# Optimization experiments

Hardware: AMD Instinct MI355X
Metric: run time of the kernel (lower is better)

Reference implementation:

```python
import jax, jax.numpy as jnp
import numpy as np

DIM = 128
LAYERS = 3
N_NODES = 50000
N_EDGES = 640000
LN_EPS = 1e-5


def setup_inputs() -> dict:
    key = jax.random.key(0)
    ks = jax.random.split(key, 10)
    s = 1.0 / np.sqrt(DIM)
    x = jax.random.normal(ks[0], (N_NODES, DIM), dtype=jnp.float32)
    edge_index = jax.random.randint(ks[1], (2, N_EDGES), 0, N_NODES, dtype=jnp.int64)
    in_w = jax.random.uniform(ks[2], (DIM, DIM), jnp.float32, -s, s)
    in_b = jax.random.uniform(ks[3], (DIM,), jnp.float32, -s, s)
    w1 = jax.random.uniform(ks[4], (LAYERS, DIM, DIM), jnp.float32, -s, s)
    b1 = jax.random.uniform(ks[5], (LAYERS, DIM), jnp.float32, -s, s)
    w2 = jax.random.uniform(ks[6], (LAYERS, DIM, DIM), jnp.float32, -s, s)
    b2 = jax.random.uniform(ks[7], (LAYERS, DIM), jnp.float32, -s, s)
    ln_g = jnp.ones((LAYERS, DIM), jnp.float32)
    ln_b = jnp.zeros((LAYERS, DIM), jnp.float32)
    return {"x": x, "edge_index": edge_index, "in_w": in_w, "in_b": in_b,
            "w1": w1, "b1": b1, "w2": w2, "b2": b2, "ln_g": ln_g, "ln_b": ln_b}


def _layer_norm(z, g, b):
    mu = jnp.mean(z, axis=-1, keepdims=True)
    var = jnp.mean(jnp.square(z - mu), axis=-1, keepdims=True)
    return (z - mu) * jax.lax.rsqrt(var + LN_EPS) * g + b


def reference(x, edge_index, in_w, in_b, w1, b1, w2, b2, ln_g, ln_b):
    src, dst = edge_index[0], edge_index[1]
    n = x.shape[0]
    # degree is identical every layer in the original; compute once (same math)
    deg = jax.ops.segment_sum(jnp.ones(dst.shape, x.dtype), dst, num_segments=n)
    deg = jnp.maximum(deg, 1.0)[:, None]  # [N,1]
    h = x @ in_w + in_b  # [N,D]
    for i in range(w1.shape[0]):
        m = jax.ops.segment_sum(h[src], dst, num_segments=n) / deg  # gather+scatter
        mlp = jax.nn.relu(m @ w1[i] + b1[i]) @ w2[i] + b2[i]
        h = _layer_norm(h + mlp, ln_g[i], ln_b[i])
    return h
```

## Files before the change

kernel.cpp:

```cpp
#include <hip/hip_runtime.h>
#include <hip/hip_fp8.h>

#define DIM 128
#define LN_EPS 1e-5f

typedef __attribute__((ext_vector_type(8))) short s16x8;
typedef __attribute__((ext_vector_type(4))) float f32x4;
typedef __attribute__((ext_vector_type(2))) float f32x2;
typedef __attribute__((ext_vector_type(4))) unsigned int u32x4;
typedef __attribute__((ext_vector_type(2))) unsigned int u32x2;

__device__ __forceinline__ unsigned short f2bf(float f) {
    unsigned u = __float_as_uint(f);
    unsigned r = u + 0x7fffu + ((u >> 16) & 1u);
    return (unsigned short)(r >> 16);
}
__device__ __forceinline__ float bf2f(unsigned short b) {
    return __uint_as_float(((unsigned)b) << 16);
}
__device__ __forceinline__ unsigned char f2fp8(float f) {
    return (unsigned char)__hip_cvt_float_to_fp8(f, __HIP_SATFINITE, __HIP_E4M3);
}
__device__ __forceinline__ void acc_fp8x4(float* a, unsigned v) {
    f32x2 lo = __builtin_amdgcn_cvt_pk_f32_fp8(v, false);
    f32x2 hi = __builtin_amdgcn_cvt_pk_f32_fp8(v, true);
    a[0] += lo[0]; a[1] += lo[1]; a[2] += hi[0]; a[3] += hi[1];
}


__global__ void count_deg(const int* __restrict__ dst, int E, int* __restrict__ counts) {
    int i = blockIdx.x * 256 + threadIdx.x;
    if (i < E) atomicAdd(&counts[dst[i]], 1);
}

__global__ __launch_bounds__(256) void scan_partials(const int* __restrict__ counts, int n,
                                                     int* __restrict__ bsum) {
    int base = blockIdx.x * 1024 + threadIdx.x * 4;
    int s = 0;
#pragma unroll
    for (int j = 0; j < 4; ++j) {
        int i = base + j;
        if (i < n) s += counts[i];
    }
#pragma unroll
    for (int off = 32; off > 0; off >>= 1) s += __shfl_xor(s, off, 64);
    __shared__ int wsum[4];
    int lane = threadIdx.x & 63, wid = threadIdx.x >> 6;
    if (lane == 0) wsum[wid] = s;
    __syncthreads();
    if (threadIdx.x == 0) bsum[blockIdx.x] = wsum[0] + wsum[1] + wsum[2] + wsum[3];
}

__global__ __launch_bounds__(64) void scan_bsums(const int* __restrict__ bsum,
                                                 int* __restrict__ bofs, int nb,
                                                 int* __restrict__ rowptr, int N, int E) {
    int lane = threadIdx.x;
    int carry = 0;
    for (int base = 0; base < nb; base += 64) {
        int v = (base + lane < nb) ? bsum[base + lane] : 0;
        int incl = v;
#pragma unroll
        for (int off = 1; off < 64; off <<= 1) {
            int t = __shfl_up(incl, off, 64);
            if (lane >= off) incl += t;
        }
        if (base + lane < nb) bofs[base + lane] = carry + incl - v;
        carry += __shfl(incl, 63, 64);
    }
    if (lane == 0) rowptr[N] = E;
}

__global__ __launch_bounds__(256) void scan_final(const int* __restrict__ counts, int n,
                                                  const int* __restrict__ bofs,
                                                  int* __restrict__ rowptr,
                                                  int* __restrict__ cursor,
                                                  float* __restrict__ dinv) {
    int base = blockIdx.x * 1024 + threadIdx.x * 4;
    int v[4];
#pragma unroll
    for (int j = 0; j < 4; ++j) {
        int i = base + j;
        v[j] = (i < n) ? counts[i] : 0;
    }
    int tsum = v[0] + v[1] + v[2] + v[3];
    int lane = threadIdx.x & 63, wid = threadIdx.x >> 6;
    int incl = tsum;
#pragma unroll
    for (int off = 1; off < 64; off <<= 1) {
        int t = __shfl_up(incl, off, 64);
        if (lane >= off) incl += t;
    }
    __shared__ int wsum[4];
    if (lane == 63) wsum[wid] = incl;
    __syncthreads();
    int wofs = 0;
    for (int w = 0; w < 4; ++w)
        if (w < wid) wofs += wsum[w];
    int excl = bofs[blockIdx.x] + wofs + (incl - tsum);
#pragma unroll
    for (int j = 0; j < 4; ++j) {
        int i = base + j;
        if (i < n) {
            rowptr[i] = excl;
            cursor[i] = excl;
            dinv[i] = 1.0f / (float)((v[j] > 1) ? v[j] : 1);
            excl += v[j];
        }
    }
}

__global__ void fill_csr(const int* __restrict__ src, const int* __restrict__ dst, int E,
                         int* __restrict__ cursor, int* __restrict__ srcidx) {
    int i = blockIdx.x * 256 + threadIdx.x;
    if (i < E) {
        int p = atomicAdd(&cursor[dst[i]], 1);
        srcidx[p] = src[i];
    }
}


__global__ __launch_bounds__(256) void cvt_weights(const float* __restrict__ in_w,
                                                   const float* __restrict__ w1,
                                                   const float* __restrict__ w2,
                                                   unsigned short* __restrict__ wt, int L) {
    int mat = blockIdx.x >> 3, part = blockIdx.x & 7;
    const float* src;
    if (mat == 0) src = in_w;
    else if (mat <= L) src = w1 + (size_t)(mat - 1) * DIM * DIM;
    else src = w2 + (size_t)(mat - 1 - L) * DIM * DIM;
    unsigned short* dst = wt + (size_t)mat * DIM * DIM;
    int base = part * 2048 + threadIdx.x;
#pragma unroll
    for (int j = 0; j < 8; ++j) {
        int i = base + j * 256;
        int k = i >> 7, n = i & 127;
        dst[n * DIM + k] = f2bf(src[i]);
    }
}


__global__ __launch_bounds__(256) void gemm_bias_mfma(const float* __restrict__ x,
                                                      const unsigned short* __restrict__ Wt,
                                                      const float* __restrict__ bias,
                                                      unsigned short* __restrict__ hb,
                                                      unsigned char* __restrict__ h8, int N) {
    int tid = threadIdx.x;
    int s = tid >> 6, lane = tid & 63;
    int quad = lane >> 4, l16 = lane & 15;
    int r0 = blockIdx.x * 16;
    int cs = s * 32;
    int arow = r0 + l16;
    bool av = arow < N;

    f32x4 acc[2];
    acc[0] = (f32x4){0.f, 0.f, 0.f, 0.f};
    acc[1] = (f32x4){0.f, 0.f, 0.f, 0.f};

    const float4* xp = (const float4*)(x + ((size_t)(av ? arow : 0) << 7)) + quad * 2;
#pragma unroll
    for (int k0 = 0; k0 < 128; k0 += 32) {
        s16x8 a = {0, 0, 0, 0, 0, 0, 0, 0};
        if (av) {
            float4 f0 = xp[k0 / 4];
            float4 f1 = xp[k0 / 4 + 1];
            a[0] = (short)f2bf(f0.x); a[1] = (short)f2bf(f0.y);
            a[2] = (short)f2bf(f0.z); a[3] = (short)f2bf(f0.w);
            a[4] = (short)f2bf(f1.x); a[5] = (short)f2bf(f1.y);
            a[6] = (short)f2bf(f1.z); a[7] = (short)f2bf(f1.w);
        }
        s16x8 b0 = *(const s16x8*)(Wt + ((size_t)(cs + l16) << 7) + quad * 8 + k0);
        s16x8 b1 = *(const s16x8*)(Wt + ((size_t)(cs + 16 + l16) << 7) + quad * 8 + k0);
        acc[0] = __builtin_amdgcn_mfma_f32_16x16x32_bf16(a, b0, acc[0], 0, 0, 0);
        acc[1] = __builtin_amdgcn_mfma_f32_16x16x32_bf16(a, b1, acc[1], 0, 0, 0);
    }

#pragma unroll
    for (int c = 0; c < 2; ++c) {
        int col = cs + c * 16 + l16;
        float bv = bias[col];
#pragma unroll
        for (int reg = 0; reg < 4; ++reg) {
            int grow = r0 + quad * 4 + reg;
            if (grow < N) {
                float o = acc[c][reg] + bv;
                hb[((size_t)grow << 7) + col] = f2bf(o);
                h8[((size_t)grow << 7) + col] = f2fp8(o);
            }
        }
    }
}


__global__ __launch_bounds__(256) void agg_mlp_ln(const unsigned short* __restrict__ hin,
                                                  const unsigned char* __restrict__ h8in,
                                                  const int* __restrict__ rowptr,
                                                  const int* __restrict__ srcidx,
                                                  const float* __restrict__ dinv,
                                                  const unsigned short* __restrict__ W1t,
                                                  const float* __restrict__ B1,
                                                  const unsigned short* __restrict__ W2t,
                                                  const float* __restrict__ B2,
                                                  const float* __restrict__ G,
                                                  const float* __restrict__ Bb,
                                                  unsigned short* __restrict__ hout,
                                                  unsigned char* __restrict__ h8out,
                                                  float* __restrict__ out_f32, int N) {
    __shared__ unsigned short M[16][132];
    __shared__ unsigned short P[16][132];
    __shared__ float s1p[4][16], s2p[4][16];

    int tid = threadIdx.x;
    int s = tid >> 6, lane = tid & 63;
    int quad = lane >> 4, l16 = lane & 15;
    int g = lane >> 2, li = lane & 3;
    int r0 = blockIdx.x * 16;
    int cs = s * 32;

    int nd = r0 + g;
    bool nv = nd < N;
    int e  = nv ? rowptr[nd] : 0;
    int ee = nv ? rowptr[nd + 1] : 0;

    float a0[8] = {0, 0, 0, 0, 0, 0, 0, 0};
    float a1[8] = {0, 0, 0, 0, 0, 0, 0, 0};
    const unsigned char* hsl = h8in + cs + li * 8;

    while (__any(e < ee)) {
        int myidx = (e + li < ee) ? srcidx[e + li] : 0;
        int i0 = __shfl(myidx, (g << 2) | 0, 64);
        int i1 = __shfl(myidx, (g << 2) | 1, 64);
        int i2 = __shfl(myidx, (g << 2) | 2, 64);
        int i3 = __shfl(myidx, (g << 2) | 3, 64);
        bool p0 = e < ee, p1 = e + 1 < ee, p2 = e + 2 < ee, p3 = e + 3 < ee;
        u32x2 v0, v1, v2, v3;
        if (p0) v0 = *(const u32x2*)(hsl + ((size_t)i0 << 7));
        if (p1) v1 = *(const u32x2*)(hsl + ((size_t)i1 << 7));
        if (p2) v2 = *(const u32x2*)(hsl + ((size_t)i2 << 7));
        if (p3) v3 = *(const u32x2*)(hsl + ((size_t)i3 << 7));
        if (p0) { acc_fp8x4(a0,     v0[0]); acc_fp8x4(a0 + 4, v0[1]); }
        if (p1) { acc_fp8x4(a1,     v1[0]); acc_fp8x4(a1 + 4, v1[1]); }
        if (p2) { acc_fp8x4(a0,     v2[0]); acc_fp8x4(a0 + 4, v2[1]); }
        if (p3) { acc_fp8x4(a1,     v3[0]); acc_fp8x4(a1 + 4, v3[1]); }
        e += 4;
    }

    {
        float di = nv ? dinv[nd] : 0.f;
        u32x4 o;
#pragma unroll
        for (int j = 0; j < 4; ++j) {
            unsigned lo = f2bf((a0[2 * j]     + a1[2 * j])     * di);
            unsigned hi = f2bf((a0[2 * j + 1] + a1[2 * j + 1]) * di);
            o[j] = lo | (hi << 16);
        }
        *(u32x4*)(&M[g][cs + li * 8]) = o;
    }
    __syncthreads();

    f32x4 acc[2];
    acc[0] = (f32x4){0.f, 0.f, 0.f, 0.f};
    acc[1] = (f32x4){0.f, 0.f, 0.f, 0.f};
#pragma unroll
    for (int k0 = 0; k0 < 128; k0 += 32) {
        s16x8 a = *(const s16x8*)(&M[l16][quad * 8 + k0]);
        s16x8 b0 = *(const s16x8*)(W1t + ((size_t)(cs + l16) << 7) + quad * 8 + k0);
        s16x8 b1 = *(const s16x8*)(W1t + ((size_t)(cs + 16 + l16) << 7) + quad * 8 + k0);
        acc[0] = __builtin_amdgcn_mfma_f32_16x16x32_bf16(a, b0, acc[0], 0, 0, 0);
        acc[1] = __builtin_amdgcn_mfma_f32_16x16x32_bf16(a, b1, acc[1], 0, 0, 0);
    }
#pragma unroll
    for (int c = 0; c < 2; ++c) {
        int col = cs + c * 16 + l16;
        float bv = B1[col];
#pragma unroll
        for (int reg = 0; reg < 4; ++reg) {
            float v = fmaxf(acc[c][reg] + bv, 0.f);
            P[quad * 4 + reg][col] = f2bf(v);
        }
    }
    __syncthreads();

    acc[0] = (f32x4){0.f, 0.f, 0.f, 0.f};
    acc[1] = (f32x4){0.f, 0.f, 0.f, 0.f};
#pragma unroll
    for (int k0 = 0; k0 < 128; k0 += 32) {
        s16x8 a = *(const s16x8*)(&P[l16][quad * 8 + k0]);
        s16x8 b0 = *(const s16x8*)(W2t + ((size_t)(cs + l16) << 7) + quad * 8 + k0);
        s16x8 b1 = *(const s16x8*)(W2t + ((size_t)(cs + 16 + l16) << 7) + quad * 8 + k0);
        acc[0] = __builtin_amdgcn_mfma_f32_16x16x32_bf16(a, b0, acc[0], 0, 0, 0);
        acc[1] = __builtin_amdgcn_mfma_f32_16x16x32_bf16(a, b1, acc[1], 0, 0, 0);
    }

    float z[2][4];
    float ps1[4] = {0, 0, 0, 0}, ps2[4] = {0, 0, 0, 0};
#pragma unroll
    for (int c = 0; c < 2; ++c) {
        int col = cs + c * 16 + l16;
        float b2v = B2[col];
#pragma unroll
        for (int reg = 0; reg < 4; ++reg) {
            int grow = r0 + quad * 4 + reg;
            float hv = (grow < N) ? bf2f(hin[((size_t)grow << 7) + col]) : 0.f;
            float zz = acc[c][reg] + b2v + hv;
            z[c][reg] = zz;
            ps1[reg] += zz;
            ps2[reg] += zz * zz;
        }
    }
#pragma unroll
    for (int off = 1; off < 16; off <<= 1) {
#pragma unroll
        for (int reg = 0; reg < 4; ++reg) {
            ps1[reg] += __shfl_xor(ps1[reg], off, 64);
            ps2[reg] += __shfl_xor(ps2[reg], off, 64);
        }
    }
    if (l16 == 0) {
#pragma unroll
        for (int reg = 0; reg < 4; ++reg) {
            s1p[s][quad * 4 + reg] = ps1[reg];
            s2p[s][quad * 4 + reg] = ps2[reg];
        }
    }
    __syncthreads();

#pragma unroll
    for (int reg = 0; reg < 4; ++reg) {
        int row = quad * 4 + reg;
        float S1 = s1p[0][row] + s1p[1][row] + s1p[2][row] + s1p[3][row];
        float S2 = s2p[0][row] + s2p[1][row] + s2p[2][row] + s2p[3][row];
        float mean = S1 * (1.0f / 128.0f);
        float var = S2 * (1.0f / 128.0f) - mean * mean;
        float rs = rsqrtf(var + LN_EPS);
        int grow = r0 + row;
        if (grow < N) {
#pragma unroll
            for (int c = 0; c < 2; ++c) {
                int col = cs + c * 16 + l16;
                float o = (z[c][reg] - mean) * rs * G[col] + Bb[col];
                if (out_f32) {
                    out_f32[((size_t)grow << 7) + col] = o;
                } else {
                    hout[((size_t)grow << 7) + col] = f2bf(o);
                    h8out[((size_t)grow << 7) + col] = f2fp8(o);
                }
            }
        }
    }
}


extern "C" void kernel_launch(void* const* d_in, const int* in_sizes, int n_in,
                              void* d_out, int out_size, void* d_ws, size_t ws_size,
                              hipStream_t stream) {
    const float* x    = (const float*)d_in[0];
    const int*   ei   = (const int*)d_in[1];
    const float* in_w = (const float*)d_in[2];
    const float* in_b = (const float*)d_in[3];
    const float* w1   = (const float*)d_in[4];
    const float* b1   = (const float*)d_in[5];
    const float* w2   = (const float*)d_in[6];
    const float* b2   = (const float*)d_in[7];
    const float* ln_g = (const float*)d_in[8];
    const float* ln_b = (const float*)d_in[9];

    const int N = in_sizes[0] / DIM;
    const int E = in_sizes[1] / 2;
    const int LAYERS = in_sizes[4] / (DIM * DIM);

    const int* e_src = ei;
    const int* e_dst = ei + E;

    char* ws = (char*)d_ws;
    unsigned short* hb0    = (unsigned short*)ws;  ws += (size_t)N * DIM * 2;
    unsigned short* hb1    = (unsigned short*)ws;  ws += (size_t)N * DIM * 2;
    unsigned char*  h8a    = (unsigned char*)ws;   ws += (size_t)N * DIM;
    unsigned char*  h8b    = (unsigned char*)ws;   ws += (size_t)N * DIM;
    int*            counts = (int*)ws;             ws += (size_t)N * 4;
    int*            rowptr = (int*)ws;             ws += (size_t)(N + 1) * 4;
    int*            cursor = (int*)ws;             ws += (size_t)N * 4;
    float*          dinv   = (float*)ws;           ws += (size_t)N * 4;
    int*            srcidx = (int*)ws;             ws += (size_t)E * 4;
    int*            bsum   = (int*)ws;             ws += 4096;
    int*            bofs   = (int*)ws;             ws += 4096;
    unsigned short* wt     = (unsigned short*)ws;  ws += (size_t)(2 * LAYERS + 1) * DIM * DIM * 2;

    const int nScanBlocks = (N + 1023) / 1024;
    const int nMat = 2 * LAYERS + 1;

    (void)hipMemsetAsync(counts, 0, (size_t)N * 4, stream);
    count_deg<<<(E + 255) / 256, 256, 0, stream>>>(e_dst, E, counts);
    scan_partials<<<nScanBlocks, 256, 0, stream>>>(counts, N, bsum);
    scan_bsums<<<1, 64, 0, stream>>>(bsum, bofs, nScanBlocks, rowptr, N, E);
    scan_final<<<nScanBlocks, 256, 0, stream>>>(counts, N, bofs, rowptr, cursor, dinv);
    fill_csr<<<(E + 255) / 256, 256, 0, stream>>>(e_src, e_dst, E, cursor, srcidx);
    cvt_weights<<<nMat * 8, 256, 0, stream>>>(in_w, w1, w2, wt, LAYERS);

    const unsigned short* in_wt = wt;
    const unsigned short* w1t   = wt + (size_t)DIM * DIM;
    const unsigned short* w2t   = wt + (size_t)(1 + LAYERS) * DIM * DIM;

    int tile_grid = (N + 15) / 16;
    gemm_bias_mfma<<<tile_grid, 256, 0, stream>>>(x, in_wt, in_b, hb0, h8a, N);

    unsigned short* hin  = hb0;  unsigned char* h8in  = h8a;
    unsigned short* hout = hb1;  unsigned char* h8out = h8b;
    for (int i = 0; i < LAYERS; ++i) {
        float* out = (i == LAYERS - 1) ? (float*)d_out : nullptr;
        agg_mlp_ln<<<tile_grid, 256, 0, stream>>>(hin, h8in, rowptr, srcidx, dinv,
                                                  w1t + (size_t)i * DIM * DIM, b1 + (size_t)i * DIM,
                                                  w2t + (size_t)i * DIM * DIM, b2 + (size_t)i * DIM,
                                                  ln_g + (size_t)i * DIM, ln_b + (size_t)i * DIM,
                                                  hout, h8out, out, N);
        unsigned short* t = hin; hin = hout; hout = t;
        unsigned char* t8 = h8in; h8in = h8out; h8out = t8;
    }
}
```

Measured before the change: 349.4 us.

## Balance edge aggregation across lanes with merge-path split and LDS atomics

Replaces the per-node gather loop, where each 4-lane group walked one destination's edges, with an even split of the block's 16-node edge range across the 16 groups. Each group may cover several nodes, so partial sums are flushed into an fp32 shared tile with LDS atomicAdd at node boundaries. The aim is to remove wavefront divergence from uneven node degrees. In exchange it adds LDS atomics, an extra zero-init pass and a bf16 conversion pass, and drops the 4-way unrolled loads, which lowers memory-level parallelism per lane.

```diff
diff --git a/kernel.cpp b/kernel.cpp
--- a/kernel.cpp
+++ b/kernel.cpp
@@ -205,9 +205,11 @@
                                                   unsigned short* __restrict__ hout,
                                                   unsigned char* __restrict__ h8out,
                                                   float* __restrict__ out_f32, int N) {
-    __shared__ unsigned short M[16][132];
+    __shared__ float Mf[16][129];
+    __shared__ unsigned short Mb[16][132];
     __shared__ unsigned short P[16][132];
     __shared__ float s1p[4][16], s2p[4][16];
+    __shared__ int rpS[17];
 
     int tid = threadIdx.x;
     int s = tid >> 6, lane = tid & 63;
@@ -216,44 +218,59 @@
     int r0 = blockIdx.x * 16;
     int cs = s * 32;
 
-    int nd = r0 + g;
-    bool nv = nd < N;
-    int e  = nv ? rowptr[nd] : 0;
-    int ee = nv ? rowptr[nd + 1] : 0;
-
-    float a0[8] = {0, 0, 0, 0, 0, 0, 0, 0};
-    float a1[8] = {0, 0, 0, 0, 0, 0, 0, 0};
-    const unsigned char* hsl = h8in + cs + li * 8;
-
-    while (__any(e < ee)) {
-        int myidx = (e + li < ee) ? srcidx[e + li] : 0;
-        int i0 = __shfl(myidx, (g << 2) | 0, 64);
-        int i1 = __shfl(myidx, (g << 2) | 1, 64);
-        int i2 = __shfl(myidx, (g << 2) | 2, 64);
-        int i3 = __shfl(myidx, (g << 2) | 3, 64);
-        bool p0 = e < ee, p1 = e + 1 < ee, p2 = e + 2 < ee, p3 = e + 3 < ee;
-        u32x2 v0, v1, v2, v3;
-        if (p0) v0 = *(const u32x2*)(hsl + ((size_t)i0 << 7));
-        if (p1) v1 = *(const u32x2*)(hsl + ((size_t)i1 << 7));
-        if (p2) v2 = *(const u32x2*)(hsl + ((size_t)i2 << 7));
-        if (p3) v3 = *(const u32x2*)(hsl + ((size_t)i3 << 7));
-        if (p0) { acc_fp8x4(a0,     v0[0]); acc_fp8x4(a0 + 4, v0[1]); }
-        if (p1) { acc_fp8x4(a1,     v1[0]); acc_fp8x4(a1 + 4, v1[1]); }
-        if (p2) { acc_fp8x4(a0,     v2[0]); acc_fp8x4(a0 + 4, v2[1]); }
-        if (p3) { acc_fp8x4(a1,     v3[0]); acc_fp8x4(a1 + 4, v3[1]); }
-        e += 4;
-    }
-
+    if (tid < 17) {
+        int idx = r0 + tid;
+        rpS[tid] = rowptr[idx < N ? idx : N];
+    }
     {
-        float di = nv ? dinv[nd] : 0.f;
-        u32x4 o;
-#pragma unroll
-        for (int j = 0; j < 4; ++j) {
-            unsigned lo = f2bf((a0[2 * j]     + a1[2 * j])     * di);
-            unsigned hi = f2bf((a0[2 * j + 1] + a1[2 * j + 1]) * di);
-            o[j] = lo | (hi << 16);
-        }
-        *(u32x4*)(&M[g][cs + li * 8]) = o;
+        int row = tid >> 4, c0 = (tid & 15) * 8;
+#pragma unroll
+        for (int k = 0; k < 8; ++k) Mf[row][c0 + k] = 0.f;
+    }
+    __syncthreads();
+
+    {
+        int eb0 = rpS[0], eb1 = rpS[16];
+        int total = eb1 - eb0;
+        int c = total >> 4, rem = total & 15;
+        int a = eb0 + g * c + (g < rem ? g : rem);
+        int b = a + c + (g < rem ? 1 : 0);
+
+        int node = 0;
+        while (node < 15 && rpS[node + 1] <= a) node++;
+        int bnd = rpS[node + 1];
+
+        float a8[8] = {0, 0, 0, 0, 0, 0, 0, 0};
+        const unsigned char* hsl = h8in + cs + li * 8;
+
+        for (int e = a; e < b; ++e) {
+            int sidx = srcidx[e];
+            u32x2 v = *(const u32x2*)(hsl + ((size_t)sidx << 7));
+            acc_fp8x4(a8, v[0]);
+            acc_fp8x4(a8 + 4, v[1]);
+            if (e + 1 == bnd || e + 1 == b) {
+#pragma unroll
+                for (int k = 0; k < 8; ++k) {
+                    atomicAdd(&Mf[node][cs + li * 8 + k], a8[k]);
+                    a8[k] = 0.f;
+                }
+                while (node < 15 && rpS[node + 1] <= e + 1) node++;
+                bnd = rpS[node + 1];
+            }
+        }
+    }
+    __syncthreads();
+
+    {
+        int row = tid >> 4, c0 = (tid & 15) * 8;
+        int nd = r0 + row;
+        float di = (nd < N) ? dinv[nd] : 0.f;
+#pragma unroll
+        for (int k = 0; k < 8; k += 2) {
+            unsigned lo = f2bf(Mf[row][c0 + k] * di);
+            unsigned hi = f2bf(Mf[row][c0 + k + 1] * di);
+            *(unsigned*)(&Mb[row][c0 + k]) = lo | (hi << 16);
+        }
     }
     __syncthreads();
 
@@ -262,7 +279,7 @@
     acc[1] = (f32x4){0.f, 0.f, 0.f, 0.f};
 #pragma unroll
     for (int k0 = 0; k0 < 128; k0 += 32) {
-        s16x8 a = *(const s16x8*)(&M[l16][quad * 8 + k0]);
+        s16x8 a = *(const s16x8*)(&Mb[l16][quad * 8 + k0]);
         s16x8 b0 = *(const s16x8*)(W1t + ((size_t)(cs + l16) << 7) + quad * 8 + k0);
         s16x8 b1 = *(const s16x8*)(W1t + ((size_t)(cs + 16 + l16) << 7) + quad * 8 + k0);
         acc[0] = __builtin_amdgcn_mfma_f32_16x16x32_bf16(a, b0, acc[0], 0, 0, 0);
```

Measured after the change: 476.8 us. 1.36x slower.

## Restructure neighbor gather so each wave handles full rows of four nodes

Applied to the files above, without the earlier changes.

The aggregation phase now gives each wavefront four destination nodes and reads full 128-byte FP8 rows. Eight lanes each load 16 bytes, and two lane groups split a node's edges by parity; their partial sums are merged with a cross-lane shuffle. Before, each wave covered a 32-column slice for all 16 nodes, so every edge index was fetched and every row touched by all four waves. The change reads each source row once, in wider 16-byte loads, and drops the index shuffles. It also widens the LDS row padding from 132 to 136, and it raises register use (two 16-float accumulators) and load imbalance between waves when node degrees differ.

```diff
diff --git a/kernel.cpp b/kernel.cpp
--- a/kernel.cpp
+++ b/kernel.cpp
@@ -205,55 +205,68 @@
                                                   unsigned short* __restrict__ hout,
                                                   unsigned char* __restrict__ h8out,
                                                   float* __restrict__ out_f32, int N) {
-    __shared__ unsigned short M[16][132];
-    __shared__ unsigned short P[16][132];
+    __shared__ unsigned short M[16][136];
+    __shared__ unsigned short P[16][136];
     __shared__ float s1p[4][16], s2p[4][16];
 
     int tid = threadIdx.x;
     int s = tid >> 6, lane = tid & 63;
     int quad = lane >> 4, l16 = lane & 15;
-    int g = lane >> 2, li = lane & 3;
     int r0 = blockIdx.x * 16;
     int cs = s * 32;
 
-    int nd = r0 + g;
-    bool nv = nd < N;
-    int e  = nv ? rowptr[nd] : 0;
-    int ee = nv ? rowptr[nd + 1] : 0;
-
-    float a0[8] = {0, 0, 0, 0, 0, 0, 0, 0};
-    float a1[8] = {0, 0, 0, 0, 0, 0, 0, 0};
-    const unsigned char* hsl = h8in + cs + li * 8;
-
-    while (__any(e < ee)) {
-        int myidx = (e + li < ee) ? srcidx[e + li] : 0;
-        int i0 = __shfl(myidx, (g << 2) | 0, 64);
-        int i1 = __shfl(myidx, (g << 2) | 1, 64);
-        int i2 = __shfl(myidx, (g << 2) | 2, 64);
-        int i3 = __shfl(myidx, (g << 2) | 3, 64);
-        bool p0 = e < ee, p1 = e + 1 < ee, p2 = e + 2 < ee, p3 = e + 3 < ee;
-        u32x2 v0, v1, v2, v3;
-        if (p0) v0 = *(const u32x2*)(hsl + ((size_t)i0 << 7));
-        if (p1) v1 = *(const u32x2*)(hsl + ((size_t)i1 << 7));
-        if (p2) v2 = *(const u32x2*)(hsl + ((size_t)i2 << 7));
-        if (p3) v3 = *(const u32x2*)(hsl + ((size_t)i3 << 7));
-        if (p0) { acc_fp8x4(a0,     v0[0]); acc_fp8x4(a0 + 4, v0[1]); }
-        if (p1) { acc_fp8x4(a1,     v1[0]); acc_fp8x4(a1 + 4, v1[1]); }
-        if (p2) { acc_fp8x4(a0,     v2[0]); acc_fp8x4(a0 + 4, v2[1]); }
-        if (p3) { acc_fp8x4(a1,     v3[0]); acc_fp8x4(a1 + 4, v3[1]); }
-        e += 4;
-    }
-
     {
+        int grp = lane >> 3;
+        int gp  = grp & 1;
+        int j   = grp >> 1;
+        int li8 = lane & 7;
+        int nd  = r0 + s * 4 + j;
+        bool nv = nd < N;
+        int beg = nv ? rowptr[nd] : 0;
+        int end = nv ? rowptr[nd + 1] : 0;
+
+        float a0[16], a1[16];
+#pragma unroll
+        for (int k = 0; k < 16; ++k) { a0[k] = 0.f; a1[k] = 0.f; }
+
+        const unsigned char* hp = h8in + li8 * 16;
+        int e = beg + gp;
+        while (__any(e < end)) {
+            bool p0 = e < end, p1 = (e + 2) < end;
+            int i0 = p0 ? srcidx[e] : 0;
+            int i1 = p1 ? srcidx[e + 2] : 0;
+            u32x4 v0, v1;
+            if (p0) v0 = *(const u32x4*)(hp + ((size_t)i0 << 7));
+            if (p1) v1 = *(const u32x4*)(hp + ((size_t)i1 << 7));
+            if (p0) {
+#pragma unroll
+                for (int w = 0; w < 4; ++w) acc_fp8x4(a0 + w * 4, v0[w]);
+            }
+            if (p1) {
+#pragma unroll
+                for (int w = 0; w < 4; ++w) acc_fp8x4(a1 + w * 4, v1[w]);
+            }
+            e += 4;
+        }
+
         float di = nv ? dinv[nd] : 0.f;
-        u32x4 o;
-#pragma unroll
-        for (int j = 0; j < 4; ++j) {
-            unsigned lo = f2bf((a0[2 * j]     + a1[2 * j])     * di);
-            unsigned hi = f2bf((a0[2 * j + 1] + a1[2 * j + 1]) * di);
-            o[j] = lo | (hi << 16);
-        }
-        *(u32x4*)(&M[g][cs + li * 8]) = o;
+        float t[16];
+#pragma unroll
+        for (int k = 0; k < 16; ++k) {
+            float v = a0[k] + a1[k];
+            v += __shfl_xor(v, 8, 64);
+            t[k] = v * di;
+        }
+        if (gp == 0) {
+            u32x4 o0, o1;
+#pragma unroll
+            for (int jj = 0; jj < 4; ++jj) {
+                o0[jj] = (unsigned)f2bf(t[2 * jj])     | ((unsigned)f2bf(t[2 * jj + 1]) << 16);
+                o1[jj] = (unsigned)f2bf(t[8 + 2 * jj]) | ((unsigned)f2bf(t[9 + 2 * jj]) << 16);
+            }
+            *(u32x4*)(&M[s * 4 + j][li8 * 16]) = o0;
+            *(u32x4*)(&M[s * 4 + j][li8 * 16 + 8]) = o1;
+        }
     }
     __syncthreads();
 
```

Result: slower. 377.6 us (+8.1%).
